# Kernel tuning notes

Hardware: AMD Instinct MI355X
Metric: run time of the kernel (lower is better)

## Reference

```python
import jax, jax.numpy as jnp
import numpy as np

B, L, D, H = 4, 2048, 512, 8
HD = D // H  # 64
MAX_REL = 4


def setup_inputs() -> dict:
    key = jax.random.key(0)
    ks = jax.random.split(key, 13)
    s = 1.0 / np.sqrt(D)
    return {
        "q": jax.random.normal(ks[0], (B, L, D), jnp.float32),
        "k": jax.random.normal(ks[1], (B, L, D), jnp.float32),
        "v": jax.random.normal(ks[2], (B, L, D), jnp.float32),
        "Wq": jax.random.normal(ks[3], (D, D), jnp.float32) * s,
        "bq": jax.random.normal(ks[4], (D,), jnp.float32) * 0.01,
        "Wk": jax.random.normal(ks[5], (D, D), jnp.float32) * s,
        "bk": jax.random.normal(ks[6], (D,), jnp.float32) * 0.01,
        "Wv": jax.random.normal(ks[7], (D, D), jnp.float32) * s,
        "bv": jax.random.normal(ks[8], (D,), jnp.float32) * 0.01,
        "Wo": jax.random.normal(ks[9], (D, D), jnp.float32) * s,
        "bo": jax.random.normal(ks[10], (D,), jnp.float32) * 0.01,
        "rel_k_table": jax.random.normal(ks[11], (2 * MAX_REL + 1, HD), jnp.float32),
        "rel_v_table": jax.random.normal(ks[12], (2 * MAX_REL + 1, HD), jnp.float32),
    }


def _to_heads(x):
    # [B, L, D] -> [B, H, L, HD]
    b, l, d = x.shape
    return x.reshape(b, l, H, d // H).transpose(0, 2, 1, 3)


def reference(q, k, v, Wq, bq, Wk, bk, Wv, bv, Wo, bo, rel_k_table, rel_v_table):
    # NOTE: in the source, the relative-attention output is overwritten by the
    # plain SDPA call immediately after, so observable math = SDPA only.
    # rel_k_table / rel_v_table are dead parameters (zero gradient).
    relu = jax.nn.relu
    qh = _to_heads(relu(q @ Wq.T + bq))  # [B,H,L,HD]
    kh = _to_heads(relu(k @ Wk.T + bk))
    vh = _to_heads(relu(v @ Wv.T + bv))
    # scale by sqrt(d_key)=sqrt(512), matching the original (not sqrt(head_dim))
    scores = jnp.einsum("bhqd,bhkd->bhqk", qh, kh) / jnp.sqrt(jnp.float32(D))
    attn = jax.nn.softmax(scores, axis=-1)
    out = jnp.einsum("bhqk,bhkd->bhqd", attn, vh)  # [B,H,L,HD]
    out = out.transpose(0, 2, 1, 3).reshape(B, L, D)
    return relu(out @ Wo.T + bo)
```

## Files before the change

### kernel.cpp

```cpp
#include <hip/hip_runtime.h>
#include <hip/hip_bf16.h>

#define B_  4
#define L_  2048
#define D_  512
#define H_  8
#define HD_ 64
#define M_  (B_ * L_)

typedef __bf16 bf16;
typedef __attribute__((ext_vector_type(8)))  __bf16 bf16x8;
typedef __attribute__((ext_vector_type(4)))  __bf16 bf16x4;
typedef __attribute__((ext_vector_type(16))) float  f32x16;

__device__ __forceinline__ f32x16 mfma32(bf16x8 a, bf16x8 b, f32x16 c) {
    return __builtin_amdgcn_mfma_f32_32x32x16_bf16(a, b, c, 0, 0, 0);
}

__device__ __forceinline__ void pack_body(const float* __restrict__ src,
                                          bf16* __restrict__ dst, int R,
                                          int m0, int k0)
{
    __shared__ __align__(16) bf16 tile[64][76];
    const int t = threadIdx.x;
#pragma unroll
    for (int rep = 0; rep < 4; rep++) {
        const int idx = rep * 256 + t;
        const int r = idx >> 4, c4 = idx & 15;
        const float4 f = *(const float4*)(src + (size_t)(m0 + r) * 512 + k0 + c4 * 4);
        bf16x4 v; v[0] = (bf16)f.x; v[1] = (bf16)f.y; v[2] = (bf16)f.z; v[3] = (bf16)f.w;
        *(bf16x4*)(&tile[r][c4 * 4]) = v;
    }
    __syncthreads();
#pragma unroll
    for (int rep = 0; rep < 2; rep++) {
        const int s = rep * 256 + t;
        const int ml = s & 63, kpl = s >> 6;
        const bf16x4 lo = *(const bf16x4*)(&tile[ml][kpl * 8]);
        const bf16x4 hi4 = *(const bf16x4*)(&tile[ml][kpl * 8 + 4]);
        bf16x8 v;
#pragma unroll
        for (int e = 0; e < 4; e++) { v[e] = lo[e]; v[e + 4] = hi4[e]; }
        *(bf16x8*)(dst + ((size_t)(k0 / 8 + kpl) * R + m0 + ml) * 8) = v;
    }
}

__global__ __launch_bounds__(256) void pack_all(
    const float* __restrict__ q, const float* __restrict__ k,
    const float* __restrict__ v,
    const float* __restrict__ W0, const float* __restrict__ W1,
    const float* __restrict__ W2, const float* __restrict__ W3,
    bf16* __restrict__ Wp, bf16* __restrict__ P0, bf16* __restrict__ P1,
    bf16* __restrict__ P2)
{
    const int z = blockIdx.z;
    if (z < 4) {
        if (blockIdx.x >= 8) return;
        const float* src = z == 0 ? W0 : z == 1 ? W1 : z == 2 ? W2 : W3;
        pack_body(src, Wp + (size_t)z * 64 * 512 * 8, 512, blockIdx.x * 64, blockIdx.y * 64);
    } else {
        const float* src = z == 4 ? q : z == 5 ? k : v;
        bf16* dst = z == 4 ? P0 : z == 5 ? P1 : P2;
        pack_body(src, dst, M_, blockIdx.x * 64, blockIdx.y * 64);
    }
}

struct PJob {
    const bf16* X; const bf16* W; const float* bias; void* out;
    float postmul; int mode;
};

__global__ __launch_bounds__(256, 3) void proj_kernel(PJob j0, PJob j1, PJob j2)
{
    const PJob jb = (blockIdx.z == 0) ? j0 : (blockIdx.z == 1) ? j1 : j2;
    const int w    = threadIdx.x >> 6;
    const int lane = threadIdx.x & 63;
    const int l31  = lane & 31;
    const int hi   = lane >> 5;
    const int m0 = blockIdx.x * 128;
    const int n0 = blockIdx.y * 64;
    const int mh = w & 1;
    const int nh = w >> 1;

    __shared__ __align__(16) bf16 Ab[2][16][64][8];
    __shared__ __align__(16) bf16 Bb[2][8][64][8];

    f32x16 acc[2];
#pragma unroll
    for (int mi = 0; mi < 2; mi++)
#pragma unroll
        for (int r = 0; r < 16; r++) acc[mi][r] = 0.0f;

    auto ldA = [&](int f, int k0) -> bf16x8 {
        return *(const bf16x8*)(jb.X + ((size_t)((k0 >> 3) + (f >> 2) * 2 + hi) * M_
                                        + m0 + (f & 3) * 32 + l31) * 8);
    };
    auto ldB = [&](int f, int k0) -> bf16x8 {
        return *(const bf16x8*)(jb.W + ((size_t)((k0 >> 3) + (f >> 1) * 2 + hi) * 512
                                        + n0 + (f & 1) * 32 + l31) * 8);
    };

    bf16x8 rA[3][4], rB[3][2];
#pragma unroll
    for (int i = 0; i < 4; i++) rA[0][i] = ldA(w * 4 + i, 0);
#pragma unroll
    for (int i = 0; i < 2; i++) rB[0][i] = ldB(w * 2 + i, 0);
#pragma unroll
    for (int i = 0; i < 4; i++) *(bf16x8*)(&Ab[0][w * 4 + i][lane][0]) = rA[0][i];
#pragma unroll
    for (int i = 0; i < 2; i++) *(bf16x8*)(&Bb[0][w * 2 + i][lane][0]) = rB[0][i];
#pragma unroll
    for (int s = 1; s < 3; s++) {
#pragma unroll
        for (int i = 0; i < 4; i++) rA[s][i] = ldA(w * 4 + i, s * 64);
#pragma unroll
        for (int i = 0; i < 2; i++) rB[s][i] = ldB(w * 2 + i, s * 64);
    }
    __syncthreads();

#pragma unroll
    for (int it = 0; it < 8; it++) {
        const int cur = it & 1;
        if (it < 5) {
            const int s = it % 3, kn = (it + 3) * 64;
#pragma unroll
            for (int i = 0; i < 4; i++) rA[s][i] = ldA(w * 4 + i, kn);
#pragma unroll
            for (int i = 0; i < 2; i++) rB[s][i] = ldB(w * 2 + i, kn);
        }
#pragma unroll
        for (int ks = 0; ks < 4; ks++) {
            const bf16x8 bfr = *(const bf16x8*)(&Bb[cur][ks * 2 + nh][lane][0]);
#pragma unroll
            for (int mi = 0; mi < 2; mi++) {
                const bf16x8 afr = *(const bf16x8*)(&Ab[cur][ks * 4 + mh * 2 + mi][lane][0]);
                acc[mi] = mfma32(afr, bfr, acc[mi]);
            }
        }
        if (it < 7) {
            const int s = (it + 1) % 3;
#pragma unroll
            for (int i = 0; i < 4; i++) *(bf16x8*)(&Ab[1 - cur][w * 4 + i][lane][0]) = rA[s][i];
#pragma unroll
            for (int i = 0; i < 2; i++) *(bf16x8*)(&Bb[1 - cur][w * 2 + i][lane][0]) = rB[s][i];
            __syncthreads();
        }
    }

    const int col = n0 + nh * 32 + l31;
    const float bn = jb.bias[col];
    const int mode = jb.mode;
#pragma unroll
    for (int mi = 0; mi < 2; mi++)
#pragma unroll
        for (int r = 0; r < 16; r++) {
            const int row = m0 + (mh * 2 + mi) * 32 + (r & 3) + 8 * (r >> 2) + 4 * hi;
            float v = fmaxf(acc[mi][r] + bn, 0.0f);
            if (mode == 2) {
                ((float*)jb.out)[(size_t)row * D_ + col] = v;
            } else {
                v *= jb.postmul;
                const int b = row >> 11, l = row & (L_ - 1);
                const int h = col >> 6,  hd = col & (HD_ - 1);
                const int bh = b * H_ + h;
                size_t idx;
                if (mode == 0) {
                    idx = ((size_t)bh * L_ + l) * HD_ + hd;
                } else if (mode == 1) {
                    idx = (((size_t)bh * 8 + (hd >> 3)) * L_ + l) * 8 + (hd & 7);
                } else {
                    const int swzl = (l & ~15) | (l & 3) | ((l & 4) << 1) | ((l & 8) >> 1);
                    idx = (((size_t)bh * 256 + (swzl >> 3)) * 64 + hd) * 8 + (swzl & 7);
                }
                ((bf16*)jb.out)[idx] = (bf16)v;
            }
        }
}

__global__ __launch_bounds__(64, 2) void attn_kernel(
    const bf16* __restrict__ qh, const bf16* __restrict__ Kp,
    const bf16* __restrict__ Vp, bf16* __restrict__ Op)
{
    const int lane = threadIdx.x;
    const int l31  = lane & 31;
    const int hi   = lane >> 5;

    const int lin  = blockIdx.x + (blockIdx.y << 6);
    const int xcd  = lin & 7;
    const int slot = lin >> 3;
    const int bh   = (xcd << 2) + (slot >> 6);
    const int qb   = (slot & 63) << 5;

    const bf16* Q   = qh + (size_t)bh * L_ * HD_;
    const bf16* Kpb = Kp + (size_t)bh * 8 * L_ * 8;
    const bf16* Vpb = Vp + (size_t)bh * 256 * 64 * 8;

    bf16x8 qf[4];
#pragma unroll
    for (int ks = 0; ks < 4; ks++)
        qf[ks] = *(const bf16x8*)(Q + (size_t)(qb + l31) * HD_ + ks * 16 + hi * 8);

    f32x16 zz;
#pragma unroll
    for (int r = 0; r < 16; r++) zz[r] = 0.0f;
    f32x16 o0 = zz, o1 = zz, lacc = zz;
    bf16x8 ones;
#pragma unroll
    for (int u = 0; u < 8; u++) ones[u] = (bf16)1.0f;

    auto ldK = [&](int f, int t) -> bf16x8 {
        return *(const bf16x8*)(Kpb + ((size_t)((f >> 1) * 2 + hi) * L_
                                       + t * 64 + (f & 1) * 32 + l31) * 8);
    };
    auto ldV = [&](int f, int t) -> bf16x8 {
        return *(const bf16x8*)(Vpb + ((size_t)(t * 8 + (f >> 1) * 2 + hi) * 64
                                       + (f & 1) * 32 + l31) * 8);
    };

    bf16x8 kr[8], vf[8];
#pragma unroll
    for (int f = 0; f < 8; f++) kr[f] = ldK(f, 0);
#pragma unroll
    for (int f = 0; f < 8; f++) vf[f] = ldV(f, 0);

#pragma unroll 2
    for (int t = 0; t < 32; t++) {
        __builtin_amdgcn_s_setprio(1);
        f32x16 s0 = mfma32(kr[0], qf[0], zz);
        f32x16 s1 = mfma32(kr[1], qf[0], zz);
#pragma unroll
        for (int ks = 1; ks < 4; ks++) {
            s0 = mfma32(kr[ks * 2 + 0], qf[ks], s0);
            s1 = mfma32(kr[ks * 2 + 1], qf[ks], s1);
        }
        __builtin_amdgcn_s_setprio(0);
        if (t < 31) {
#pragma unroll
            for (int f = 0; f < 8; f++) kr[f] = ldK(f, t + 1);
        }

#pragma unroll
        for (int r = 0; r < 16; r++) s0[r] = __builtin_amdgcn_exp2f(s0[r]);
        bf16x8 pf0, pf1;
#pragma unroll
        for (int u = 0; u < 8; u++) { pf0[u] = (bf16)s0[u]; pf1[u] = (bf16)s0[8 + u]; }
        __builtin_amdgcn_s_setprio(1);
        o0   = mfma32(pf0, vf[0], o0);
        o1   = mfma32(pf0, vf[1], o1);
        lacc = mfma32(pf0, ones, lacc);
        o0   = mfma32(pf1, vf[2], o0);
        o1   = mfma32(pf1, vf[3], o1);
        lacc = mfma32(pf1, ones, lacc);
        __builtin_amdgcn_s_setprio(0);
        if (t < 31) {
#pragma unroll
            for (int f = 0; f < 4; f++) vf[f] = ldV(f, t + 1);
        }

#pragma unroll
        for (int r = 0; r < 16; r++) s1[r] = __builtin_amdgcn_exp2f(s1[r]);
        bf16x8 pf2, pf3;
#pragma unroll
        for (int u = 0; u < 8; u++) { pf2[u] = (bf16)s1[u]; pf3[u] = (bf16)s1[8 + u]; }
        __builtin_amdgcn_s_setprio(1);
        o0   = mfma32(pf2, vf[4], o0);
        o1   = mfma32(pf2, vf[5], o1);
        lacc = mfma32(pf2, ones, lacc);
        o0   = mfma32(pf3, vf[6], o0);
        o1   = mfma32(pf3, vf[7], o1);
        lacc = mfma32(pf3, ones, lacc);
        __builtin_amdgcn_s_setprio(0);
        if (t < 31) {
#pragma unroll
            for (int f = 4; f < 8; f++) vf[f] = ldV(f, t + 1);
        }
    }

    const int b = bh >> 3, h = bh & 7;
#pragma unroll
    for (int r = 0; r < 16; r++) {
        const int rl = (r & 3) + 8 * (r >> 2) + 4 * hi;
        const float inv = 1.0f / lacc[r];
        const int m = b * L_ + qb + rl;
        const int c0 = h * HD_ + l31;
        Op[((size_t)(c0 >> 3) * M_ + m) * 8 + (c0 & 7)] = (bf16)(o0[r] * inv);
        const int c1 = c0 + 32;
        Op[((size_t)(c1 >> 3) * M_ + m) * 8 + (c1 & 7)] = (bf16)(o1[r] * inv);
    }
}

extern "C" void kernel_launch(void* const* d_in, const int* in_sizes, int n_in,
                              void* d_out, int out_size, void* d_ws, size_t ws_size,
                              hipStream_t stream)
{
    (void)in_sizes; (void)n_in; (void)out_size;
    const float* q  = (const float*)d_in[0];
    const float* k  = (const float*)d_in[1];
    const float* v  = (const float*)d_in[2];
    const float* Wq = (const float*)d_in[3];
    const float* bq = (const float*)d_in[4];
    const float* Wk = (const float*)d_in[5];
    const float* bk = (const float*)d_in[6];
    const float* Wv = (const float*)d_in[7];
    const float* bv = (const float*)d_in[8];
    const float* Wo = (const float*)d_in[9];
    const float* bo = (const float*)d_in[10];
    float* out = (float*)d_out;

    char* ws = (char*)d_ws;
    const size_t MB = 1024 * 1024;
    bf16* P0  = (bf16*)(ws);
    bf16* P1  = (bf16*)(ws + 8 * MB);
    bf16* P2  = (bf16*)(ws + 16 * MB);
    bf16* Wp  = (bf16*)(ws + 24 * MB);
    bf16* qh  = (bf16*)(d_out);
    bf16* Kp  = (bf16*)((char*)d_out + 8 * MB);
    bf16* Opb = P1;

    bf16* Wqp = Wp;
    bf16* Wkp = Wp + (size_t)64 * 512 * 8;
    bf16* Wvp = Wp + (size_t)2 * 64 * 512 * 8;
    bf16* Wop = Wp + (size_t)3 * 64 * 512 * 8;

    const float SCALE_LOG2E = 0.06377946282349575f;

    dim3 pb(256);
    pack_all<<<dim3(128, 8, 7), pb, 0, stream>>>(q, k, v, Wq, Wk, Wv, Wo,
                                                 Wp, P0, P1, P2);

    if (ws_size >= (size_t)34 * MB) {
        bf16* VpN = (bf16*)(ws + 26 * MB);
        PJob jq{P0, Wqp, bq, qh,  SCALE_LOG2E, 0};
        PJob jk{P1, Wkp, bk, Kp,  1.0f, 1};
        PJob jv{P2, Wvp, bv, VpN, 1.0f, 3};
        proj_kernel<<<dim3(64, 8, 3), pb, 0, stream>>>(jq, jk, jv);

        attn_kernel<<<dim3(64, 32), dim3(64), 0, stream>>>(qh, Kp, VpN, Opb);
    } else {
        bf16* Vp = P0;
        PJob jq{P0, Wqp, bq, qh, SCALE_LOG2E, 0};
        PJob jk{P1, Wkp, bk, Kp, 1.0f, 1};
        proj_kernel<<<dim3(64, 8, 2), pb, 0, stream>>>(jq, jk, jk);

        PJob jv{P2, Wvp, bv, Vp, 1.0f, 3};
        proj_kernel<<<dim3(64, 8, 1), pb, 0, stream>>>(jv, jv, jv);

        attn_kernel<<<dim3(64, 32), dim3(64), 0, stream>>>(qh, Kp, Vp, Opb);
    }

    PJob jo{Opb, Wop, bo, out, 1.0f, 2};
    proj_kernel<<<dim3(64, 8, 1), pb, 0, stream>>>(jo, jo, jo);
}
```

Before: 202.5 us.

## Split attention key range across two waves per block and reduce via LDS

The attention kernel now launches two 64-lane waves per block. Each wave processes half of the key/value tiles for the same 32-query block, and the partial output and row-sum accumulators are combined through shared memory. The goal is to double the number of waves in flight (2048 blocks with one wave each before, now two waves each) so the MFMA and load latency of the long sequential key loop is hidden better. In exchange it adds an LDS write/read, a block barrier, and an idle wave during the epilogue.

```diff
diff --git a/kernel.cpp b/kernel.cpp
--- a/kernel.cpp
+++ b/kernel.cpp
@@ -177,13 +177,15 @@
         }
 }
 
-__global__ __launch_bounds__(64, 2) void attn_kernel(
+__global__ __launch_bounds__(128, 4) void attn_kernel(
     const bf16* __restrict__ qh, const bf16* __restrict__ Kp,
     const bf16* __restrict__ Vp, bf16* __restrict__ Op)
 {
-    const int lane = threadIdx.x;
+    const int w    = threadIdx.x >> 6;
+    const int lane = threadIdx.x & 63;
     const int l31  = lane & 31;
     const int hi   = lane >> 5;
+    const int tw   = w * 16;
 
     const int lin  = blockIdx.x + (blockIdx.y << 6);
     const int xcd  = lin & 7;
@@ -194,6 +196,8 @@
     const bf16* Q   = qh + (size_t)bh * L_ * HD_;
     const bf16* Kpb = Kp + (size_t)bh * 8 * L_ * 8;
     const bf16* Vpb = Vp + (size_t)bh * 256 * 64 * 8;
+
+    __shared__ __align__(16) float sm[3][64][16];
 
     bf16x8 qf[4];
 #pragma unroll
@@ -219,12 +223,13 @@
 
     bf16x8 kr[8], vf[8];
 #pragma unroll
-    for (int f = 0; f < 8; f++) kr[f] = ldK(f, 0);
-#pragma unroll
-    for (int f = 0; f < 8; f++) vf[f] = ldV(f, 0);
+    for (int f = 0; f < 8; f++) kr[f] = ldK(f, tw);
+#pragma unroll
+    for (int f = 0; f < 8; f++) vf[f] = ldV(f, tw);
 
 #pragma unroll 2
-    for (int t = 0; t < 32; t++) {
+    for (int tt = 0; tt < 16; tt++) {
+        const int t = tw + tt;
         __builtin_amdgcn_s_setprio(1);
         f32x16 s0 = mfma32(kr[0], qf[0], zz);
         f32x16 s1 = mfma32(kr[1], qf[0], zz);
@@ -234,7 +239,7 @@
             s1 = mfma32(kr[ks * 2 + 1], qf[ks], s1);
         }
         __builtin_amdgcn_s_setprio(0);
-        if (t < 31) {
+        if (tt < 15) {
 #pragma unroll
             for (int f = 0; f < 8; f++) kr[f] = ldK(f, t + 1);
         }
@@ -252,7 +257,7 @@
         o1   = mfma32(pf1, vf[3], o1);
         lacc = mfma32(pf1, ones, lacc);
         __builtin_amdgcn_s_setprio(0);
-        if (t < 31) {
+        if (tt < 15) {
 #pragma unroll
             for (int f = 0; f < 4; f++) vf[f] = ldV(f, t + 1);
         }
@@ -270,9 +275,26 @@
         o1   = mfma32(pf3, vf[7], o1);
         lacc = mfma32(pf3, ones, lacc);
         __builtin_amdgcn_s_setprio(0);
-        if (t < 31) {
+        if (tt < 15) {
 #pragma unroll
             for (int f = 4; f < 8; f++) vf[f] = ldV(f, t + 1);
+        }
+    }
+
+    if (w == 1) {
+        *(f32x16*)(&sm[0][lane][0]) = o0;
+        *(f32x16*)(&sm[1][lane][0]) = o1;
+        *(f32x16*)(&sm[2][lane][0]) = lacc;
+    }
+    __syncthreads();
+    if (w == 1) return;
+    {
+        const f32x16 a0 = *(const f32x16*)(&sm[0][lane][0]);
+        const f32x16 a1 = *(const f32x16*)(&sm[1][lane][0]);
+        const f32x16 al = *(const f32x16*)(&sm[2][lane][0]);
+#pragma unroll
+        for (int r = 0; r < 16; r++) {
+            o0[r] += a0[r]; o1[r] += a1[r]; lacc[r] += al[r];
         }
     }
 
@@ -335,7 +357,7 @@
         PJob jv{P2, Wvp, bv, VpN, 1.0f, 3};
         proj_kernel<<<dim3(64, 8, 3), pb, 0, stream>>>(jq, jk, jv);
 
-        attn_kernel<<<dim3(64, 32), dim3(64), 0, stream>>>(qh, Kp, VpN, Opb);
+        attn_kernel<<<dim3(64, 32), dim3(128), 0, stream>>>(qh, Kp, VpN, Opb);
     } else {
         bf16* Vp = P0;
         PJob jq{P0, Wqp, bq, qh, SCALE_LOG2E, 0};
@@ -345,7 +367,7 @@
         PJob jv{P2, Wvp, bv, Vp, 1.0f, 3};
         proj_kernel<<<dim3(64, 8, 1), pb, 0, stream>>>(jv, jv, jv);
 
-        attn_kernel<<<dim3(64, 32), dim3(64), 0, stream>>>(qh, Kp, Vp, Opb);
+        attn_kernel<<<dim3(64, 32), dim3(128), 0, stream>>>(qh, Kp, Vp, Opb);
     }
 
     PJob jo{Opb, Wop, bo, out, 1.0f, 2};
```

Measured after the change: 617.8 us. 3.05x slower.
